# Kernel optimization log

Measured on AMD Instinct MI355X. Metric: run time of the kernel, lower is better.

The kernel has to match this reference:

```python
import math
import jax, jax.numpy as jnp
from jax import lax
import numpy as np

N, C, H, W = 32, 256, 56, 56

def setup_inputs() -> dict:
    key = jax.random.key(0)
    k = jax.random.split(key, 5)
    return {
        "x": jax.random.normal(k[0], (N, C, H, W), dtype=jnp.float32),
        "p1_w": jax.random.normal(k[1], (H, W, C, 1), dtype=jnp.float32) * 0.1,
        "conv_w": jax.random.normal(k[2], (C, C // 2, 3, 3), dtype=jnp.float32) * 0.05,
        "p4_w": jax.random.normal(k[3], (1, C, C), dtype=jnp.float32) * 0.1,
        "p5_w": jax.random.normal(k[4], (C, 1), dtype=jnp.float32) * 0.1,
    }

def reference(x, p1_w, conv_w, p4_w, p5_w):
    n, c, h, w = x.shape
    inv_sqrt_c = 1.0 / math.sqrt(c)
    # t_1: einsum 'abcd,cdef->abef' -> [n, c, c, 1] -> [n, c, c]
    t1 = jnp.einsum('nchw,hwef->ncef', x, p1_w)[..., 0]
    # t_3: grouped 3x3 conv, groups=2, no bias -> [n, c, h, w]
    t3 = lax.conv_general_dilated(
        x, conv_w, window_strides=(1, 1), padding=((1, 1), (1, 1)),
        dimension_numbers=('NCHW', 'OIHW', 'NCHW'), feature_group_count=2)
    # t_4: broadcast elementwise scale [1,c,c] * [n,c,c]
    t4 = p4_w * t1
    # t_5: [n,c,c] @ [c,1] -> [n,c]
    t5 = jnp.einsum('nab,bo->nao', t4, p5_w)[..., 0]
    # t_6: bmm(t4 [n,c,c], t3 [n,c,hw]) / sqrt(c) -> [n,c,h,w]
    t6 = (jnp.einsum('nab,nbs->nas', t4, t3.reshape(n, c, h * w))
          .reshape(n, c, h, w)) * inv_sqrt_c
    # t_7: bmm(t5 [n,1,c], x [n,c,hw]) / sqrt(c) -> [n,h,w]
    t7 = (jnp.einsum('nc,ncs->ns', t5, x.reshape(n, c, h * w))
          .reshape(n, h, w)) * inv_sqrt_c
    # t_8: broadcast add [n,1,h,w] + [n,c,h,w]
    return t7[:, None, :, :] + t6
```

## Files before the change

### kernel.cpp

```cpp
#include <hip/hip_runtime.h>

#define HWB   3136
#define HWPAD 3200
#define SPAD  3364

typedef __attribute__((ext_vector_type(8))) short bf16x8;
typedef __attribute__((ext_vector_type(4))) float f32x4;

__device__ __forceinline__ unsigned short f2bf(float f) {
    unsigned u = __float_as_uint(f);
    unsigned r = (u + 0x7fffu + ((u >> 16) & 1u)) >> 16;
    return (unsigned short)r;
}
__device__ __forceinline__ float bf2f(unsigned short h) {
    return __uint_as_float(((unsigned)h) << 16);
}
__device__ __forceinline__ void gl_lds16(const void* g, void* l) {
    __builtin_amdgcn_global_load_lds(
        (const __attribute__((address_space(1))) void*)g,
        (__attribute__((address_space(3))) void*)l, 16, 0, 0);
}

__global__ __launch_bounds__(256) void k_prep(
    const float* __restrict__ x, unsigned short* __restrict__ xc,
    unsigned short* __restrict__ xp)
{
    __shared__ short tile[64 * 66];
    const int n = blockIdx.z, c0 = blockIdx.y * 64, s0 = blockIdx.x * 64;
    const int t = threadIdx.x;
    const int cl = t >> 2;
    const int sq = (t & 3) * 16;

    const float* src = x + ((size_t)(n * 256 + c0 + cl)) * HWB + s0 + sq;
    unsigned short bf[16];
#pragma unroll
    for (int j = 0; j < 4; ++j) {
        float4 v = *(const float4*)(src + j * 4);
        bf[j * 4 + 0] = f2bf(v.x); bf[j * 4 + 1] = f2bf(v.y);
        bf[j * 4 + 2] = f2bf(v.z); bf[j * 4 + 3] = f2bf(v.w);
    }
    unsigned short* xcb = xc + ((size_t)(n * 256 + c0 + cl)) * HWB + s0 + sq;
    *(bf16x8*)xcb = *(const bf16x8*)&bf[0];
    *(bf16x8*)(xcb + 8) = *(const bf16x8*)&bf[8];
#pragma unroll
    for (int k = 0; k < 16; ++k)
        tile[(sq + k) * 66 + cl] = (short)bf[k];
    __syncthreads();
    const int r = t >> 2;
    const int cq = (t & 3) * 16;
    unsigned short ob[16];
#pragma unroll
    for (int j = 0; j < 8; ++j) {
        unsigned w = *(const unsigned*)&tile[r * 66 + cq + 2 * j];
        ob[2 * j] = (unsigned short)w;
        ob[2 * j + 1] = (unsigned short)(w >> 16);
    }
    const int s = s0 + r;
    const int sp = s + 2 * (s / 56) + 59;
    unsigned short* dst = xp + ((size_t)n * SPAD + sp) * 256 + c0 + cq;
    *(bf16x8*)dst = *(const bf16x8*)&ob[0];
    *(bf16x8*)(dst + 8) = *(const bf16x8*)&ob[8];
}

__global__ __launch_bounds__(256) void k_zero(
    unsigned short* __restrict__ xp)
{
    const int n = blockIdx.y;
    const int idx = blockIdx.x * 256 + threadIdx.x;
    if (idx >= 228 * 32) return;
    const int i = idx >> 5, ch = idx & 31;
    int sp;
    if (i < 58)       sp = i;
    else if (i < 116) sp = 3306 + (i - 58);
    else if (i < 172) sp = (i - 115) * 58;
    else              sp = (i - 171) * 58 + 57;
    bf16x8 z = {};
    *(bf16x8*)&xp[((size_t)n * SPAD + sp) * 256 + ch * 8] = z;
}

__global__ __launch_bounds__(256) void k_prep_p1t(
    const float* __restrict__ p1, unsigned short* __restrict__ p1t)
{
    __shared__ unsigned short tile[32][33];
    const int e0 = blockIdx.y * 32, h0 = blockIdx.x * 32;
    const int lx = threadIdx.x & 31, ly = threadIdx.x >> 5;
#pragma unroll
    for (int it = 0; it < 4; ++it) {
        int lh = ly + it * 8;
        tile[lh][lx] = f2bf(p1[(size_t)(h0 + lh) * 256 + e0 + lx]);
    }
    __syncthreads();
#pragma unroll
    for (int it = 0; it < 4; ++it) {
        int le = ly + it * 8;
        p1t[(size_t)(e0 + le) * HWB + h0 + lx] = tile[lx][le];
    }
}

__global__ __launch_bounds__(256) void k_prep_w(
    const float* __restrict__ w, unsigned short* __restrict__ wp)
{
    const int o = blockIdx.x, t = threadIdx.x;
#pragma unroll
    for (int k = t; k < 1152; k += 256) {
        int tap = k >> 7, ci = k & 127;
        wp[(size_t)o * 1152 + k] = f2bf(w[(size_t)o * 1152 + ci * 9 + tap]);
    }
}

__global__ __launch_bounds__(256) void k_conv(
    const unsigned short* __restrict__ xp, const unsigned short* __restrict__ wp,
    unsigned short* __restrict__ t3cl)
{
    __shared__ short As[2][128 * 64];
    __shared__ short Bs[2][128 * 64];
    const int tid = threadIdx.x;
    const int orig = blockIdx.x;
    const int wgid = (orig & 7) * 200 + (orig >> 3);
    const int ng = wgid / 25;
    const int tileS = (wgid - ng * 25) * 128;
    const int n = ng >> 1, g = ng & 1;
    const int wave = tid >> 6, lane = tid & 63;
    const int wm = (wave >> 1) * 64, wn = (wave & 1) * 64;

    const int rl = tid >> 3, q = tid & 7;
    const int swq = (q ^ (rl & 7)) * 8;

    const unsigned short* xpn = xp + (size_t)n * SPAD * 256 + g * 128 + swq;
    const unsigned short* arow[4];
    const unsigned short* brow[4];
#pragma unroll
    for (int p = 0; p < 4; ++p) {
        int s = tileS + p * 32 + rl;
        int sc = s < HWB ? s : HWB - 1;
        int sp = sc + 2 * (sc / 56) + 59;
        arow[p] = xpn + (size_t)sp * 256;
        brow[p] = wp + (size_t)(g * 128 + p * 32 + rl) * 1152 + swq;
    }

    f32x4 acc[4][4] = {};
    const int frow = lane & 15, quad = lane >> 4, sw = frow & 7;
    int rofA[4], rofB[4];
#pragma unroll
    for (int i = 0; i < 4; ++i) {
        rofA[i] = (wm + i * 16 + frow) * 64;
        rofB[i] = (wn + i * 16 + frow) * 64;
    }
    const int ldst = (tid >> 3) * 64 + (tid & 7) * 8;

    {
        const int shift0 = (-59) * 256;
#pragma unroll
        for (int p = 0; p < 4; ++p) {
            gl_lds16(arow[p] + shift0, &As[0][p * 2048 + ldst]);
            gl_lds16(brow[p], &Bs[0][p * 2048 + ldst]);
        }
    }
    __syncthreads();

    int cur = 0;
#pragma unroll
    for (int t = 0; t < 18; ++t) {
        if (t < 17) {
            const int tn = t + 1;
            const int tap = tn >> 1;
            const int shift = ((tap / 3 - 1) * 58 + (tap % 3 - 1)) * 256 + (tn & 1) * 64;
#pragma unroll
            for (int p = 0; p < 4; ++p) {
                gl_lds16(arow[p] + shift, &As[cur ^ 1][p * 2048 + ldst]);
                gl_lds16(brow[p] + tn * 64, &Bs[cur ^ 1][p * 2048 + ldst]);
            }
        }
        const short* Ab = As[cur];
        const short* Bb = Bs[cur];
#pragma unroll
        for (int h = 0; h < 2; ++h) {
            bf16x8 af[4], bfr[4];
#pragma unroll
            for (int i = 0; i < 4; ++i)
                af[i] = *(const bf16x8*)&Ab[rofA[i] + ((h * 4 + quad) ^ sw) * 8];
#pragma unroll
            for (int j = 0; j < 4; ++j)
                bfr[j] = *(const bf16x8*)&Bb[rofB[j] + ((h * 4 + quad) ^ sw) * 8];
#pragma unroll
            for (int i = 0; i < 4; ++i)
#pragma unroll
                for (int j = 0; j < 4; ++j)
                    acc[i][j] = __builtin_amdgcn_mfma_f32_16x16x32_bf16(af[i], bfr[j], acc[i][j], 0, 0, 0);
        }
        __syncthreads();
        cur ^= 1;
    }
    unsigned short* ob = t3cl + (size_t)n * HWPAD * 256 + g * 128;
#pragma unroll
    for (int i = 0; i < 4; ++i)
#pragma unroll
        for (int r = 0; r < 4; ++r) {
            int s = tileS + wm + i * 16 + (lane >> 4) * 4 + r;
            int c = wn + (lane & 15);
#pragma unroll
            for (int j = 0; j < 4; ++j) {
                float v = (s < HWB) ? acc[i][j][r] : 0.f;
                ob[(size_t)s * 256 + c + j * 16] = f2bf(v);
            }
        }
}

__global__ __launch_bounds__(256) void k_gemm1(
    const unsigned short* __restrict__ xc, const unsigned short* __restrict__ p1t,
    float* __restrict__ part)
{
    __shared__ short As[2][128 * 64];
    __shared__ short Bs[2][128 * 64];
    const int tid = threadIdx.x;
    const int orig = blockIdx.x;
    const int wgid = (orig & 7) * 64 + (orig >> 3);
    const int z = wgid >> 7;
    const int rem = wgid & 127;
    const int tileM = (rem >> 1) * 128;
    const int tileN = (rem & 1) * 128;
    const int kbase = z ? (832 + (z - 1) * 768) : 0;
    const int nk = z ? 12 : 13;
    const int wave = tid >> 6, lane = tid & 63;
    const int wm = (wave >> 1) * 64, wn = (wave & 1) * 64;

    const int rl = tid >> 3, q = tid & 7;
    const int swq = (q ^ (rl & 7)) * 8;
    const unsigned short* asrc = xc + (size_t)(tileM + rl) * HWB + kbase + swq;
    const unsigned short* bsrc = p1t + (size_t)(tileN + rl) * HWB + kbase + swq;

    f32x4 acc[4][4] = {};
    const int frow = lane & 15, quad = lane >> 4, sw = frow & 7;
    const int ldst = rl * 64 + q * 8;

#pragma unroll
    for (int p = 0; p < 4; ++p) {
        gl_lds16(asrc + (size_t)(p * 32) * HWB, &As[0][p * 2048 + ldst]);
        gl_lds16(bsrc + (size_t)(p * 32) * HWB, &Bs[0][p * 2048 + ldst]);
    }
    __syncthreads();

    int cur = 0;
    for (int i2 = 0; i2 < nk; ++i2) {
        if (i2 + 1 < nk) {
            const int kn = (i2 + 1) * 64;
#pragma unroll
            for (int p = 0; p < 4; ++p) {
                gl_lds16(asrc + (size_t)(p * 32) * HWB + kn, &As[cur ^ 1][p * 2048 + ldst]);
                gl_lds16(bsrc + (size_t)(p * 32) * HWB + kn, &Bs[cur ^ 1][p * 2048 + ldst]);
            }
        }
        const short* Ab = As[cur];
        const short* Bb = Bs[cur];
#pragma unroll
        for (int h = 0; h < 2; ++h) {
            bf16x8 af[4], bfr[4];
#pragma unroll
            for (int i = 0; i < 4; ++i)
                af[i] = *(const bf16x8*)&Ab[(wm + i * 16 + frow) * 64 + ((h * 4 + quad) ^ sw) * 8];
#pragma unroll
            for (int j = 0; j < 4; ++j)
                bfr[j] = *(const bf16x8*)&Bb[(wn + j * 16 + frow) * 64 + ((h * 4 + quad) ^ sw) * 8];
#pragma unroll
            for (int i = 0; i < 4; ++i)
#pragma unroll
                for (int j = 0; j < 4; ++j)
                    acc[i][j] = __builtin_amdgcn_mfma_f32_16x16x32_bf16(af[i], bfr[j], acc[i][j], 0, 0, 0);
        }
        __syncthreads();
        cur ^= 1;
    }
    float* ob = part + (size_t)z * 8192 * 256;
#pragma unroll
    for (int j = 0; j < 4; ++j) {
        const int e = tileN + wn + j * 16 + (lane & 15);
#pragma unroll
        for (int i = 0; i < 4; ++i)
#pragma unroll
            for (int r = 0; r < 4; ++r) {
                int m = tileM + wm + i * 16 + (lane >> 4) * 4 + r;
                ob[(size_t)m * 256 + e] = acc[i][j][r];
            }
    }
}

__global__ __launch_bounds__(256) void k_t4scale(
    const float* __restrict__ part, const float* __restrict__ p4,
    const float* __restrict__ p5, unsigned short* __restrict__ t4h,
    float* __restrict__ t5)
{
    const int row = blockIdx.x * 4 + (threadIdx.x >> 6);
    const int lane = threadIdx.x & 63;
    const size_t off = (size_t)row * 256 + lane * 4;
    const size_t slab = (size_t)8192 * 256;
    float4 a0 = *(const float4*)&part[off];
    float4 a1 = *(const float4*)&part[off + slab];
    float4 a2 = *(const float4*)&part[off + 2 * slab];
    float4 a3 = *(const float4*)&part[off + 3 * slab];
    float4 a;
    a.x = (a0.x + a1.x) + (a2.x + a3.x);
    a.y = (a0.y + a1.y) + (a2.y + a3.y);
    a.z = (a0.z + a1.z) + (a2.z + a3.z);
    a.w = (a0.w + a1.w) + (a2.w + a3.w);
    float4 sc = *(const float4*)&p4[(size_t)(row & 255) * 256 + lane * 4];
    float4 pv = *(const float4*)&p5[lane * 4];
    float v0 = a.x * sc.x, v1 = a.y * sc.y, v2 = a.z * sc.z, v3 = a.w * sc.w;
    ushort4 o;
    o.x = f2bf(v0); o.y = f2bf(v1); o.z = f2bf(v2); o.w = f2bf(v3);
    *(ushort4*)&t4h[(size_t)row * 256 + lane * 4] = o;
    float sum = v0 * pv.x + v1 * pv.y + v2 * pv.z + v3 * pv.w;
#pragma unroll
    for (int offd = 32; offd > 0; offd >>= 1) sum += __shfl_down(sum, offd);
    if (lane == 0) t5[row] = sum;
}

__global__ __launch_bounds__(256) void k_t7(
    const unsigned short* __restrict__ xc, const float* __restrict__ t5,
    float* __restrict__ t7)
{
    const int n = blockIdx.z;
    const int c0 = blockIdx.y * 32;
    const int s0 = blockIdx.x * 1568;
    __shared__ float wv[32];
    const int t = threadIdx.x;
    if (t < 32) wv[t] = t5[n * 256 + c0 + t];
    __syncthreads();
    if (t >= 196) return;
    const unsigned short* base = xc + ((size_t)(n * 256 + c0)) * HWB + s0 + t * 8;
    float acc[8] = {};
    for (int c = 0; c < 32; ++c) {
        bf16x8 v = *(const bf16x8*)(base + (size_t)c * HWB);
        float w = wv[c];
#pragma unroll
        for (int j = 0; j < 8; ++j)
            acc[j] += w * bf2f((unsigned short)v[j]);
    }
    float* dst = t7 + (size_t)n * HWB + s0 + t * 8;
#pragma unroll
    for (int j = 0; j < 8; ++j)
        atomicAdd(&dst[j], acc[j] * 0.0625f);
}

__global__ __launch_bounds__(256) void k_bmm(
    const unsigned short* __restrict__ t4h, const unsigned short* __restrict__ t3cl,
    const float* __restrict__ t7, float* __restrict__ out)
{
    __shared__ short As[2][128 * 64];
    __shared__ short Bs[2][128 * 64];
    const int tid = threadIdx.x;
    const int orig = blockIdx.x;
    const int wgid = (orig & 7) * 200 + (orig >> 3);
    const int n = wgid / 50;
    const int rem = wgid - n * 50;
    const int tileA = (rem / 25) * 128;
    const int tileS = (rem % 25) * 128;
    const int wave = tid >> 6, lane = tid & 63;
    const int wm = (wave >> 1) * 64, wn = (wave & 1) * 64;

    const int rl = tid >> 3, q = tid & 7;
    const int swq = (q ^ (rl & 7)) * 8;
    const unsigned short* asrc = t4h + ((size_t)n * 256 + tileA + rl) * 256 + swq;
    const unsigned short* bsrc = t3cl + ((size_t)n * HWPAD + tileS + rl) * 256 + swq;

    f32x4 acc[4][4] = {};
    const int frow = lane & 15, quad = lane >> 4, sw = frow & 7;
    const int ldst = rl * 64 + q * 8;

#pragma unroll
    for (int p = 0; p < 4; ++p) {
        gl_lds16(asrc + (size_t)(p * 32) * 256, &As[0][p * 2048 + ldst]);
        gl_lds16(bsrc + (size_t)(p * 32) * 256, &Bs[0][p * 2048 + ldst]);
    }
    __syncthreads();

    int cur = 0;
#pragma unroll
    for (int k0 = 0; k0 < 256; k0 += 64) {
        if (k0 < 192) {
            const int kn = k0 + 64;
#pragma unroll
            for (int p = 0; p < 4; ++p) {
                gl_lds16(asrc + (size_t)(p * 32) * 256 + kn, &As[cur ^ 1][p * 2048 + ldst]);
                gl_lds16(bsrc + (size_t)(p * 32) * 256 + kn, &Bs[cur ^ 1][p * 2048 + ldst]);
            }
        }
        const short* Ab = As[cur];
        const short* Bb = Bs[cur];
#pragma unroll
        for (int h = 0; h < 2; ++h) {
            bf16x8 af[4], bfr[4];
#pragma unroll
            for (int i = 0; i < 4; ++i)
                af[i] = *(const bf16x8*)&Ab[(wm + i * 16 + frow) * 64 + ((h * 4 + quad) ^ sw) * 8];
#pragma unroll
            for (int j = 0; j < 4; ++j)
                bfr[j] = *(const bf16x8*)&Bb[(wn + j * 16 + frow) * 64 + ((h * 4 + quad) ^ sw) * 8];
#pragma unroll
            for (int i = 0; i < 4; ++i)
#pragma unroll
                for (int j = 0; j < 4; ++j)
                    acc[i][j] = __builtin_amdgcn_mfma_f32_16x16x32_bf16(af[i], bfr[j], acc[i][j], 0, 0, 0);
        }
        __syncthreads();
        cur ^= 1;
    }
    const float* t7n = t7 + (size_t)n * HWB;
    float* ob = out + (size_t)n * 256 * HWB;
#pragma unroll
    for (int j = 0; j < 4; ++j) {
        int s = tileS + wn + j * 16 + (lane & 15);
        bool vsx = s < HWB;
        float t7v = vsx ? t7n[s] : 0.f;
        if (!vsx) continue;
#pragma unroll
        for (int i = 0; i < 4; ++i)
#pragma unroll
            for (int r = 0; r < 4; ++r) {
                int a = tileA + wm + i * 16 + (lane >> 4) * 4 + r;
                ob[(size_t)a * HWB + s] = acc[i][j][r] * 0.0625f + t7v;
            }
    }
}

extern "C" void kernel_launch(void* const* d_in, const int* in_sizes, int n_in,
                              void* d_out, int out_size, void* d_ws, size_t ws_size,
                              hipStream_t stream) {
    const float* x  = (const float*)d_in[0];
    const float* p1 = (const float*)d_in[1];
    const float* cw = (const float*)d_in[2];
    const float* p4 = (const float*)d_in[3];
    const float* p5 = (const float*)d_in[4];

    char* w = (char*)d_ws;
    unsigned short* xp    = (unsigned short*)w;  w += (size_t)32 * SPAD * 256 * 2;
    unsigned short* t3cl  = (unsigned short*)w;  w += (size_t)32 * HWPAD * 256 * 2;
    unsigned short* p1t   = (unsigned short*)w;  w += (size_t)256 * HWB * 2;
    unsigned short* wpack = (unsigned short*)w;  w += (size_t)256 * 1152 * 2;
    unsigned short* t4h   = (unsigned short*)w;  w += (size_t)8192 * 256 * 2;
    float* t5             = (float*)w;           w += (size_t)8192 * 4;
    float* t7             = (float*)w;           w += (size_t)32 * HWB * 4;

    char* o = (char*)d_out;
    unsigned short* xc = (unsigned short*)o;
    float* part        = (float*)(o + (size_t)32 * 256 * HWB * 2);
    float* out = (float*)d_out;

    hipMemsetAsync(t7, 0, (size_t)32 * HWB * 4, stream);
    k_prep    <<<dim3(49, 4, 32), 256, 0, stream>>>(x, xc, xp);
    k_zero    <<<dim3(29, 32),    256, 0, stream>>>(xp);
    k_prep_p1t<<<dim3(98, 8),     256, 0, stream>>>(p1, p1t);
    k_prep_w  <<<dim3(256),       256, 0, stream>>>(cw, wpack);
    k_conv    <<<dim3(1600),      256, 0, stream>>>(xp, wpack, t3cl);
    k_gemm1   <<<dim3(512),       256, 0, stream>>>(xc, p1t, part);
    k_t4scale <<<dim3(2048),      256, 0, stream>>>(part, p4, p5, t4h, t5);
    k_t7      <<<dim3(2, 8, 32),  256, 0, stream>>>(xc, t5, t7);
    k_bmm     <<<dim3(1600),      256, 0, stream>>>(t4h, t3cl, t7, out);
}
```

Measured before the change: 369.4 us.

## Fuse grouped conv into bmm kernel, keeping t3 tile in LDS

Merges the grouped 3x3 conv and the t4·t3 batched matmul into one kernel. Each workgroup computes both conv groups for a 128-pixel tile, stores the bf16 result in a swizzled LDS buffer, then multiplies by all 256 rows of t4. This removes the t3 round-trip through global memory and one launch. The cost is 128KB of LDS per block, which lowers occupancy to one block per CU. The block count is also halved, with more serial work per block.

```diff
diff --git a/kernel.cpp b/kernel.cpp
--- a/kernel.cpp
+++ b/kernel.cpp
@@ -106,104 +106,6 @@
         int tap = k >> 7, ci = k & 127;
         wp[(size_t)o * 1152 + k] = f2bf(w[(size_t)o * 1152 + ci * 9 + tap]);
     }
-}
-
-__global__ __launch_bounds__(256) void k_conv(
-    const unsigned short* __restrict__ xp, const unsigned short* __restrict__ wp,
-    unsigned short* __restrict__ t3cl)
-{
-    __shared__ short As[2][128 * 64];
-    __shared__ short Bs[2][128 * 64];
-    const int tid = threadIdx.x;
-    const int orig = blockIdx.x;
-    const int wgid = (orig & 7) * 200 + (orig >> 3);
-    const int ng = wgid / 25;
-    const int tileS = (wgid - ng * 25) * 128;
-    const int n = ng >> 1, g = ng & 1;
-    const int wave = tid >> 6, lane = tid & 63;
-    const int wm = (wave >> 1) * 64, wn = (wave & 1) * 64;
-
-    const int rl = tid >> 3, q = tid & 7;
-    const int swq = (q ^ (rl & 7)) * 8;
-
-    const unsigned short* xpn = xp + (size_t)n * SPAD * 256 + g * 128 + swq;
-    const unsigned short* arow[4];
-    const unsigned short* brow[4];
-#pragma unroll
-    for (int p = 0; p < 4; ++p) {
-        int s = tileS + p * 32 + rl;
-        int sc = s < HWB ? s : HWB - 1;
-        int sp = sc + 2 * (sc / 56) + 59;
-        arow[p] = xpn + (size_t)sp * 256;
-        brow[p] = wp + (size_t)(g * 128 + p * 32 + rl) * 1152 + swq;
-    }
-
-    f32x4 acc[4][4] = {};
-    const int frow = lane & 15, quad = lane >> 4, sw = frow & 7;
-    int rofA[4], rofB[4];
-#pragma unroll
-    for (int i = 0; i < 4; ++i) {
-        rofA[i] = (wm + i * 16 + frow) * 64;
-        rofB[i] = (wn + i * 16 + frow) * 64;
-    }
-    const int ldst = (tid >> 3) * 64 + (tid & 7) * 8;
-
-    {
-        const int shift0 = (-59) * 256;
-#pragma unroll
-        for (int p = 0; p < 4; ++p) {
-            gl_lds16(arow[p] + shift0, &As[0][p * 2048 + ldst]);
-            gl_lds16(brow[p], &Bs[0][p * 2048 + ldst]);
-        }
-    }
-    __syncthreads();
-
-    int cur = 0;
-#pragma unroll
-    for (int t = 0; t < 18; ++t) {
-        if (t < 17) {
-            const int tn = t + 1;
-            const int tap = tn >> 1;
-            const int shift = ((tap / 3 - 1) * 58 + (tap % 3 - 1)) * 256 + (tn & 1) * 64;
-#pragma unroll
-            for (int p = 0; p < 4; ++p) {
-                gl_lds16(arow[p] + shift, &As[cur ^ 1][p * 2048 + ldst]);
-                gl_lds16(brow[p] + tn * 64, &Bs[cur ^ 1][p * 2048 + ldst]);
-            }
-        }
-        const short* Ab = As[cur];
-        const short* Bb = Bs[cur];
-#pragma unroll
-        for (int h = 0; h < 2; ++h) {
-            bf16x8 af[4], bfr[4];
-#pragma unroll
-            for (int i = 0; i < 4; ++i)
-                af[i] = *(const bf16x8*)&Ab[rofA[i] + ((h * 4 + quad) ^ sw) * 8];
-#pragma unroll
-            for (int j = 0; j < 4; ++j)
-                bfr[j] = *(const bf16x8*)&Bb[rofB[j] + ((h * 4 + quad) ^ sw) * 8];
-#pragma unroll
-            for (int i = 0; i < 4; ++i)
-#pragma unroll
-                for (int j = 0; j < 4; ++j)
-                    acc[i][j] = __builtin_amdgcn_mfma_f32_16x16x32_bf16(af[i], bfr[j], acc[i][j], 0, 0, 0);
-        }
-        __syncthreads();
-        cur ^= 1;
-    }
-    unsigned short* ob = t3cl + (size_t)n * HWPAD * 256 + g * 128;
-#pragma unroll
-    for (int i = 0; i < 4; ++i)
-#pragma unroll
-        for (int r = 0; r < 4; ++r) {
-            int s = tileS + wm + i * 16 + (lane >> 4) * 4 + r;
-            int c = wn + (lane & 15);
-#pragma unroll
-            for (int j = 0; j < 4; ++j) {
-                float v = (s < HWB) ? acc[i][j][r] : 0.f;
-                ob[(size_t)s * 256 + c + j * 16] = f2bf(v);
-            }
-        }
 }
 
 __global__ __launch_bounds__(256) void k_gemm1(
@@ -341,83 +243,160 @@
         atomicAdd(&dst[j], acc[j] * 0.0625f);
 }
 
-__global__ __launch_bounds__(256) void k_bmm(
-    const unsigned short* __restrict__ t4h, const unsigned short* __restrict__ t3cl,
-    const float* __restrict__ t7, float* __restrict__ out)
-{
-    __shared__ short As[2][128 * 64];
-    __shared__ short Bs[2][128 * 64];
+__global__ __launch_bounds__(256) void k_convbmm(
+    const unsigned short* __restrict__ xp, const unsigned short* __restrict__ wp,
+    const unsigned short* __restrict__ t4h, const float* __restrict__ t7,
+    float* __restrict__ out)
+{
+    __shared__ short stg[32768];
+    __shared__ short t3t[32768];
     const int tid = threadIdx.x;
     const int orig = blockIdx.x;
-    const int wgid = (orig & 7) * 200 + (orig >> 3);
-    const int n = wgid / 50;
-    const int rem = wgid - n * 50;
-    const int tileA = (rem / 25) * 128;
-    const int tileS = (rem % 25) * 128;
+    const int wgid = (orig & 7) * 100 + (orig >> 3);
+    const int n = wgid / 25;
+    const int tileS = (wgid - n * 25) * 128;
     const int wave = tid >> 6, lane = tid & 63;
-    const int wm = (wave >> 1) * 64, wn = (wave & 1) * 64;
 
     const int rl = tid >> 3, q = tid & 7;
     const int swq = (q ^ (rl & 7)) * 8;
-    const unsigned short* asrc = t4h + ((size_t)n * 256 + tileA + rl) * 256 + swq;
-    const unsigned short* bsrc = t3cl + ((size_t)n * HWPAD + tileS + rl) * 256 + swq;
-
-    f32x4 acc[4][4] = {};
+    const int ldst = rl * 64 + q * 8;
     const int frow = lane & 15, quad = lane >> 4, sw = frow & 7;
-    const int ldst = rl * 64 + q * 8;
-
+
+    const int wm = (wave >> 1) * 64, wn = (wave & 1) * 64;
+    int rofA[4], rofB[4];
+#pragma unroll
+    for (int i = 0; i < 4; ++i) {
+        rofA[i] = (wm + i * 16 + frow) * 64;
+        rofB[i] = (wn + i * 16 + frow) * 64;
+    }
+    int sp4[4];
 #pragma unroll
     for (int p = 0; p < 4; ++p) {
-        gl_lds16(asrc + (size_t)(p * 32) * 256, &As[0][p * 2048 + ldst]);
-        gl_lds16(bsrc + (size_t)(p * 32) * 256, &Bs[0][p * 2048 + ldst]);
-    }
+        int s = tileS + p * 32 + rl;
+        int sc = s < HWB ? s : HWB - 1;
+        sp4[p] = sc + 2 * (sc / 56) + 59;
+    }
+
+    for (int g = 0; g < 2; ++g) {
+        const unsigned short* xpn = xp + (size_t)n * SPAD * 256 + g * 128 + swq;
+        const unsigned short* arow[4];
+        const unsigned short* brow[4];
+#pragma unroll
+        for (int p = 0; p < 4; ++p) {
+            arow[p] = xpn + (size_t)sp4[p] * 256;
+            brow[p] = wp + (size_t)(g * 128 + p * 32 + rl) * 1152 + swq;
+        }
+        f32x4 acc[4][4] = {};
+        {
+            const int shift0 = (-59) * 256;
+#pragma unroll
+            for (int p = 0; p < 4; ++p) {
+                gl_lds16(arow[p] + shift0, &stg[p * 2048 + ldst]);
+                gl_lds16(brow[p], &stg[16384 + p * 2048 + ldst]);
+            }
+        }
+        __syncthreads();
+        int cur = 0;
+#pragma unroll
+        for (int t = 0; t < 18; ++t) {
+            if (t < 17) {
+                const int tn = t + 1;
+                const int tap = tn >> 1;
+                const int shift = ((tap / 3 - 1) * 58 + (tap % 3 - 1)) * 256 + (tn & 1) * 64;
+#pragma unroll
+                for (int p = 0; p < 4; ++p) {
+                    gl_lds16(arow[p] + shift, &stg[(cur ^ 1) * 8192 + p * 2048 + ldst]);
+                    gl_lds16(brow[p] + tn * 64, &stg[16384 + (cur ^ 1) * 8192 + p * 2048 + ldst]);
+                }
+            }
+            const short* Ab = &stg[cur * 8192];
+            const short* Bb = &stg[16384 + cur * 8192];
+#pragma unroll
+            for (int h = 0; h < 2; ++h) {
+                bf16x8 af[4], bfr[4];
+#pragma unroll
+                for (int i = 0; i < 4; ++i)
+                    af[i] = *(const bf16x8*)&Ab[rofA[i] + ((h * 4 + quad) ^ sw) * 8];
+#pragma unroll
+                for (int j = 0; j < 4; ++j)
+                    bfr[j] = *(const bf16x8*)&Bb[rofB[j] + ((h * 4 + quad) ^ sw) * 8];
+#pragma unroll
+                for (int i = 0; i < 4; ++i)
+#pragma unroll
+                    for (int j = 0; j < 4; ++j)
+                        acc[i][j] = __builtin_amdgcn_mfma_f32_16x16x32_bf16(af[i], bfr[j], acc[i][j], 0, 0, 0);
+            }
+            __syncthreads();
+            cur ^= 1;
+        }
+#pragma unroll
+        for (int i = 0; i < 4; ++i)
+#pragma unroll
+            for (int r = 0; r < 4; ++r) {
+                const int sLoc = wm + i * 16 + quad * 4 + r;
+                const bool vs = (tileS + sLoc) < HWB;
+                const int key = sLoc & 7;
+#pragma unroll
+                for (int j = 0; j < 4; ++j) {
+                    const int oc = g * 128 + wn + j * 16 + frow;
+                    const int addr = sLoc * 256 + (((oc >> 3) ^ key) << 3) + (oc & 7);
+                    t3t[addr] = (short)f2bf(vs ? acc[i][j][r] : 0.f);
+                }
+            }
+    }
+
+    const int wm2 = wave * 64;
+    f32x4 acc2[4][8] = {};
+    const unsigned short* a2src = t4h + ((size_t)n * 256 + rl) * 256 + swq;
+
+#pragma unroll
+    for (int p = 0; p < 8; ++p)
+        gl_lds16(a2src + (size_t)(p * 32) * 256, &stg[p * 2048 + ldst]);
     __syncthreads();
 
-    int cur = 0;
+    int d = 0;
 #pragma unroll
     for (int k0 = 0; k0 < 256; k0 += 64) {
         if (k0 < 192) {
-            const int kn = k0 + 64;
-#pragma unroll
-            for (int p = 0; p < 4; ++p) {
-                gl_lds16(asrc + (size_t)(p * 32) * 256 + kn, &As[cur ^ 1][p * 2048 + ldst]);
-                gl_lds16(bsrc + (size_t)(p * 32) * 256 + kn, &Bs[cur ^ 1][p * 2048 + ldst]);
-            }
-        }
-        const short* Ab = As[cur];
-        const short* Bb = Bs[cur];
+#pragma unroll
+            for (int p = 0; p < 8; ++p)
+                gl_lds16(a2src + (size_t)(p * 32) * 256 + k0 + 64,
+                         &stg[(d ^ 1) * 16384 + p * 2048 + ldst]);
+        }
+        const short* Ab2 = &stg[d * 16384];
 #pragma unroll
         for (int h = 0; h < 2; ++h) {
-            bf16x8 af[4], bfr[4];
+            const int kc8 = (k0 >> 3) + h * 4 + quad;
+            bf16x8 af[4], bfr[8];
 #pragma unroll
             for (int i = 0; i < 4; ++i)
-                af[i] = *(const bf16x8*)&Ab[(wm + i * 16 + frow) * 64 + ((h * 4 + quad) ^ sw) * 8];
-#pragma unroll
-            for (int j = 0; j < 4; ++j)
-                bfr[j] = *(const bf16x8*)&Bb[(wn + j * 16 + frow) * 64 + ((h * 4 + quad) ^ sw) * 8];
+                af[i] = *(const bf16x8*)&Ab2[(wm2 + i * 16 + frow) * 64 + ((h * 4 + quad) ^ sw) * 8];
+#pragma unroll
+            for (int j = 0; j < 8; ++j)
+                bfr[j] = *(const bf16x8*)&t3t[(j * 16 + frow) * 256 + ((kc8 ^ sw) << 3)];
 #pragma unroll
             for (int i = 0; i < 4; ++i)
 #pragma unroll
-                for (int j = 0; j < 4; ++j)
-                    acc[i][j] = __builtin_amdgcn_mfma_f32_16x16x32_bf16(af[i], bfr[j], acc[i][j], 0, 0, 0);
+                for (int j = 0; j < 8; ++j)
+                    acc2[i][j] = __builtin_amdgcn_mfma_f32_16x16x32_bf16(af[i], bfr[j], acc2[i][j], 0, 0, 0);
         }
         __syncthreads();
-        cur ^= 1;
-    }
+        d ^= 1;
+    }
+
     const float* t7n = t7 + (size_t)n * HWB;
     float* ob = out + (size_t)n * 256 * HWB;
 #pragma unroll
-    for (int j = 0; j < 4; ++j) {
-        int s = tileS + wn + j * 16 + (lane & 15);
-        bool vsx = s < HWB;
-        float t7v = vsx ? t7n[s] : 0.f;
-        if (!vsx) continue;
+    for (int j = 0; j < 8; ++j) {
+        const int s = tileS + j * 16 + frow;
+        if (s >= HWB) continue;
+        const float t7v = t7n[s];
 #pragma unroll
         for (int i = 0; i < 4; ++i)
 #pragma unroll
             for (int r = 0; r < 4; ++r) {
-                int a = tileA + wm + i * 16 + (lane >> 4) * 4 + r;
-                ob[(size_t)a * HWB + s] = acc[i][j][r] * 0.0625f + t7v;
+                const int a = wm2 + i * 16 + quad * 4 + r;
+                ob[(size_t)a * HWB + s] = acc2[i][j][r] * 0.0625f + t7v;
             }
     }
 }
@@ -433,7 +412,6 @@
 
     char* w = (char*)d_ws;
     unsigned short* xp    = (unsigned short*)w;  w += (size_t)32 * SPAD * 256 * 2;
-    unsigned short* t3cl  = (unsigned short*)w;  w += (size_t)32 * HWPAD * 256 * 2;
     unsigned short* p1t   = (unsigned short*)w;  w += (size_t)256 * HWB * 2;
     unsigned short* wpack = (unsigned short*)w;  w += (size_t)256 * 1152 * 2;
     unsigned short* t4h   = (unsigned short*)w;  w += (size_t)8192 * 256 * 2;
@@ -450,9 +428,8 @@
     k_zero    <<<dim3(29, 32),    256, 0, stream>>>(xp);
     k_prep_p1t<<<dim3(98, 8),     256, 0, stream>>>(p1, p1t);
     k_prep_w  <<<dim3(256),       256, 0, stream>>>(cw, wpack);
-    k_conv    <<<dim3(1600),      256, 0, stream>>>(xp, wpack, t3cl);
     k_gemm1   <<<dim3(512),       256, 0, stream>>>(xc, p1t, part);
     k_t4scale <<<dim3(2048),      256, 0, stream>>>(part, p4, p5, t4h, t5);
     k_t7      <<<dim3(2, 8, 32),  256, 0, stream>>>(xc, t5, t7);
-    k_bmm     <<<dim3(1600),      256, 0, stream>>>(t4h, t3cl, t7, out);
-}
+    k_convbmm <<<dim3(800),       256, 0, stream>>>(xp, wpack, t4h, t7, out);
+}
```

Measured after the change: 405.5 us. 1.1x slower.

## Merge prep kernels and fold t7 reduction into bmm epilogue

Applied to the files above, without the earlier changes.

Combines the p1 transpose, conv-weight pack and halo-zero kernels into one launch, with branches chosen by block index. It also removes the separate t7 kernel, the memset and the atomics: each bmm workgroup now computes t7 for its 128 spatial positions from the padded channel-last x buffer and t5, and keeps the values in LDS. This cuts launch count and global round trips. In exchange, every bmm block redoes the t7 dot product, repeated across the two A-tiles, and this adds scalar work that overlaps with the first tile loads.

```diff
diff --git a/kernel.cpp b/kernel.cpp
--- a/kernel.cpp
+++ b/kernel.cpp
@@ -62,49 +62,48 @@
     *(bf16x8*)(dst + 8) = *(const bf16x8*)&ob[8];
 }
 
-__global__ __launch_bounds__(256) void k_zero(
+__global__ __launch_bounds__(256) void k_misc(
+    const float* __restrict__ p1, const float* __restrict__ cw,
+    unsigned short* __restrict__ p1t, unsigned short* __restrict__ wp,
     unsigned short* __restrict__ xp)
 {
-    const int n = blockIdx.y;
-    const int idx = blockIdx.x * 256 + threadIdx.x;
-    if (idx >= 228 * 32) return;
-    const int i = idx >> 5, ch = idx & 31;
-    int sp;
-    if (i < 58)       sp = i;
-    else if (i < 116) sp = 3306 + (i - 58);
-    else if (i < 172) sp = (i - 115) * 58;
-    else              sp = (i - 171) * 58 + 57;
-    bf16x8 z = {};
-    *(bf16x8*)&xp[((size_t)n * SPAD + sp) * 256 + ch * 8] = z;
-}
-
-__global__ __launch_bounds__(256) void k_prep_p1t(
-    const float* __restrict__ p1, unsigned short* __restrict__ p1t)
-{
-    __shared__ unsigned short tile[32][33];
-    const int e0 = blockIdx.y * 32, h0 = blockIdx.x * 32;
-    const int lx = threadIdx.x & 31, ly = threadIdx.x >> 5;
-#pragma unroll
-    for (int it = 0; it < 4; ++it) {
-        int lh = ly + it * 8;
-        tile[lh][lx] = f2bf(p1[(size_t)(h0 + lh) * 256 + e0 + lx]);
-    }
-    __syncthreads();
-#pragma unroll
-    for (int it = 0; it < 4; ++it) {
-        int le = ly + it * 8;
-        p1t[(size_t)(e0 + le) * HWB + h0 + lx] = tile[lx][le];
-    }
-}
-
-__global__ __launch_bounds__(256) void k_prep_w(
-    const float* __restrict__ w, unsigned short* __restrict__ wp)
-{
-    const int o = blockIdx.x, t = threadIdx.x;
-#pragma unroll
-    for (int k = t; k < 1152; k += 256) {
-        int tap = k >> 7, ci = k & 127;
-        wp[(size_t)o * 1152 + k] = f2bf(w[(size_t)o * 1152 + ci * 9 + tap]);
+    const int b = blockIdx.x, t = threadIdx.x;
+    if (b < 784) {
+        __shared__ unsigned short tile[32][33];
+        const int h0 = (b % 98) * 32, e0 = (b / 98) * 32;
+        const int lx = t & 31, ly = t >> 5;
+#pragma unroll
+        for (int it = 0; it < 4; ++it) {
+            int lh = ly + it * 8;
+            tile[lh][lx] = f2bf(p1[(size_t)(h0 + lh) * 256 + e0 + lx]);
+        }
+        __syncthreads();
+#pragma unroll
+        for (int it = 0; it < 4; ++it) {
+            int le = ly + it * 8;
+            p1t[(size_t)(e0 + le) * HWB + h0 + lx] = tile[lx][le];
+        }
+    } else if (b < 1040) {
+        const int o = b - 784;
+#pragma unroll
+        for (int k = t; k < 1152; k += 256) {
+            int tap = k >> 7, ci = k & 127;
+            wp[(size_t)o * 1152 + k] = f2bf(cw[(size_t)o * 1152 + ci * 9 + tap]);
+        }
+    } else {
+        const int bb = b - 1040;
+        const int n = bb / 29, xb = bb - n * 29;
+        const int idx = xb * 256 + t;
+        if (idx < 228 * 32) {
+            const int i = idx >> 5, ch = idx & 31;
+            int sp;
+            if (i < 58)       sp = i;
+            else if (i < 116) sp = 3306 + (i - 58);
+            else if (i < 172) sp = (i - 115) * 58;
+            else              sp = (i - 171) * 58 + 57;
+            bf16x8 z = {};
+            *(bf16x8*)&xp[((size_t)n * SPAD + sp) * 256 + ch * 8] = z;
+        }
     }
 }
 
@@ -314,39 +313,15 @@
     if (lane == 0) t5[row] = sum;
 }
 
-__global__ __launch_bounds__(256) void k_t7(
-    const unsigned short* __restrict__ xc, const float* __restrict__ t5,
-    float* __restrict__ t7)
-{
-    const int n = blockIdx.z;
-    const int c0 = blockIdx.y * 32;
-    const int s0 = blockIdx.x * 1568;
-    __shared__ float wv[32];
-    const int t = threadIdx.x;
-    if (t < 32) wv[t] = t5[n * 256 + c0 + t];
-    __syncthreads();
-    if (t >= 196) return;
-    const unsigned short* base = xc + ((size_t)(n * 256 + c0)) * HWB + s0 + t * 8;
-    float acc[8] = {};
-    for (int c = 0; c < 32; ++c) {
-        bf16x8 v = *(const bf16x8*)(base + (size_t)c * HWB);
-        float w = wv[c];
-#pragma unroll
-        for (int j = 0; j < 8; ++j)
-            acc[j] += w * bf2f((unsigned short)v[j]);
-    }
-    float* dst = t7 + (size_t)n * HWB + s0 + t * 8;
-#pragma unroll
-    for (int j = 0; j < 8; ++j)
-        atomicAdd(&dst[j], acc[j] * 0.0625f);
-}
-
 __global__ __launch_bounds__(256) void k_bmm(
     const unsigned short* __restrict__ t4h, const unsigned short* __restrict__ t3cl,
-    const float* __restrict__ t7, float* __restrict__ out)
+    const unsigned short* __restrict__ xp, const float* __restrict__ t5,
+    float* __restrict__ out)
 {
     __shared__ short As[2][128 * 64];
     __shared__ short Bs[2][128 * 64];
+    __shared__ float t5s[256];
+    __shared__ float t7loc[128];
     const int tid = threadIdx.x;
     const int orig = blockIdx.x;
     const int wgid = (orig & 7) * 200 + (orig >> 3);
@@ -366,6 +341,7 @@
     const int frow = lane & 15, quad = lane >> 4, sw = frow & 7;
     const int ldst = rl * 64 + q * 8;
 
+    t5s[tid] = t5[n * 256 + tid];
 #pragma unroll
     for (int p = 0; p < 4; ++p) {
         gl_lds16(asrc + (size_t)(p * 32) * 256, &As[0][p * 2048 + ldst]);
@@ -373,6 +349,23 @@
     }
     __syncthreads();
 
+    if (tid < 128) {
+        const int s = tileS + tid;
+        float accv = 0.f;
+        if (s < HWB) {
+            const int sp = s + 2 * (s / 56) + 59;
+            const unsigned short* row = xp + ((size_t)n * SPAD + sp) * 256;
+#pragma unroll
+            for (int j = 0; j < 32; ++j) {
+                bf16x8 v = *(const bf16x8*)(row + j * 8);
+#pragma unroll
+                for (int k = 0; k < 8; ++k)
+                    accv += t5s[j * 8 + k] * bf2f((unsigned short)v[k]);
+            }
+        }
+        t7loc[tid] = accv * 0.0625f;
+    }
+
     int cur = 0;
 #pragma unroll
     for (int k0 = 0; k0 < 256; k0 += 64) {
@@ -404,14 +397,13 @@
         __syncthreads();
         cur ^= 1;
     }
-    const float* t7n = t7 + (size_t)n * HWB;
     float* ob = out + (size_t)n * 256 * HWB;
 #pragma unroll
     for (int j = 0; j < 4; ++j) {
-        int s = tileS + wn + j * 16 + (lane & 15);
-        bool vsx = s < HWB;
-        float t7v = vsx ? t7n[s] : 0.f;
-        if (!vsx) continue;
+        const int sLoc = wn + j * 16 + (lane & 15);
+        const int s = tileS + sLoc;
+        if (s >= HWB) continue;
+        const float t7v = t7loc[sLoc];
 #pragma unroll
         for (int i = 0; i < 4; ++i)
 #pragma unroll
@@ -438,21 +430,16 @@
     unsigned short* wpack = (unsigned short*)w;  w += (size_t)256 * 1152 * 2;
     unsigned short* t4h   = (unsigned short*)w;  w += (size_t)8192 * 256 * 2;
     float* t5             = (float*)w;           w += (size_t)8192 * 4;
-    float* t7             = (float*)w;           w += (size_t)32 * HWB * 4;
 
     char* o = (char*)d_out;
     unsigned short* xc = (unsigned short*)o;
     float* part        = (float*)(o + (size_t)32 * 256 * HWB * 2);
     float* out = (float*)d_out;
 
-    hipMemsetAsync(t7, 0, (size_t)32 * HWB * 4, stream);
+    k_misc    <<<dim3(1968),      256, 0, stream>>>(p1, cw, p1t, wpack, xp);
     k_prep    <<<dim3(49, 4, 32), 256, 0, stream>>>(x, xc, xp);
-    k_zero    <<<dim3(29, 32),    256, 0, stream>>>(xp);
-    k_prep_p1t<<<dim3(98, 8),     256, 0, stream>>>(p1, p1t);
-    k_prep_w  <<<dim3(256),       256, 0, stream>>>(cw, wpack);
     k_conv    <<<dim3(1600),      256, 0, stream>>>(xp, wpack, t3cl);
     k_gemm1   <<<dim3(512),       256, 0, stream>>>(xc, p1t, part);
     k_t4scale <<<dim3(2048),      256, 0, stream>>>(part, p4, p5, t4h, t5);
-    k_t7      <<<dim3(2, 8, 32),  256, 0, stream>>>(xc, t5, t7);
-    k_bmm     <<<dim3(1600),      256, 0, stream>>>(t4h, t3cl, t7, out);
-}
+    k_bmm     <<<dim3(1600),      256, 0, stream>>>(t4h, t3cl, xp, t5, out);
+}
```

Result: faster. 344.6 us (-6.7%).
